# Kernel tuning notes

Hardware: AMD Instinct MI355X
Metric: run time of the kernel (lower is better)

## Reference

```python
import jax, jax.numpy as jnp
import numpy as np

B, N, D = 8, 2048, 256
K = 16384  # codebook_size


def setup_inputs() -> dict:
    key = jax.random.key(0)
    k1, k2, k3, k4 = jax.random.split(key, 4)
    z = jax.random.normal(k1, (B, N, D), dtype=jnp.float32)
    emb_weight = jax.random.normal(k2, (K, D), dtype=jnp.float32) * 0.02
    proj_w = jax.random.normal(k3, (D, D), dtype=jnp.float32) * (1.0 / np.sqrt(D))
    proj_b = jax.random.normal(k4, (D,), dtype=jnp.float32) * 0.01
    return {"z": z, "emb_weight": emb_weight, "proj_w": proj_w, "proj_b": proj_b}


def reference(z, emb_weight, proj_w, proj_b):
    # emb = embedding_proj(embedding.weight)  (torch Linear: x @ W^T + b)
    emb = emb_weight @ proj_w.T + proj_b  # (K, D)
    b, n, d = z.shape
    zf = z.reshape(b * n, d)  # (BN, D)
    # squared euclidean distances: ||z||^2 + ||e||^2 - 2 z e^T
    dist = (
        jnp.sum(zf * zf, axis=1, keepdims=True)
        + jnp.sum(emb * emb, axis=1)
        - 2.0 * jnp.einsum("bd,kd->bk", zf, emb)
    )  # (BN, K)
    q_indices = jnp.argmin(dist, axis=1)  # (BN,) int
    quantized = emb[q_indices].reshape(z.shape)  # (B, N, D)
    # straight-through estimator
    quantized = z + jax.lax.stop_gradient(quantized - z)
    q_indices = q_indices.reshape(b, n)
    # (unregularized_z, emb, regularized_z, bottleneck_rep)
    return z, emb, quantized, q_indices
```

## Files before the change

kernel.cpp:

```cpp
#include <hip/hip_runtime.h>
#include <hip/hip_bf16.h>

#define D      256
#define KCB    16384
#define BNROWS 16384
#define NT     4
#define MARGIN 0.15f
#define BIAS   8.0f
#define ZMAX   5.0f
#define EMAX   0.2f

typedef __attribute__((ext_vector_type(4))) int   int4v;
typedef __attribute__((ext_vector_type(4))) float f32x4;
typedef unsigned long long u64;

__device__ __forceinline__ void gload_lds16(const void* g, void* l) {
    __builtin_amdgcn_global_load_lds(
        (const __attribute__((address_space(1))) void*)g,
        (__attribute__((address_space(3))) void*)l, 16, 0, 0);
}

__device__ __forceinline__ unsigned fmap(float f) {
    unsigned u = __float_as_uint(f);
    return (u & 0x80000000u) ? ~u : (u | 0x80000000u);
}

__device__ __forceinline__ signed char q8(float x, float s) {
    return (signed char)__float2int_rn(fminf(fmaxf(x * s, -127.f), 127.f));
}

__global__ __launch_bounds__(256) void zquant_kernel(
    const float* __restrict__ z, signed char* __restrict__ z8)
{
    const int i = blockIdx.x * 256 + threadIdx.x;
    float4 v = ((const float4*)z)[i];
    const float s = 127.0f / ZMAX;
    char4 c;
    c.x = q8(v.x, s); c.y = q8(v.y, s); c.z = q8(v.z, s); c.w = q8(v.w, s);
    ((char4*)z8)[i] = c;
}

__global__ __launch_bounds__(256) void proj_kernel(
    const float* __restrict__ ew, const float* __restrict__ pw,
    const float* __restrict__ pb, float* __restrict__ emb)
{
    __shared__ float Et[64][65];
    __shared__ float Pt[64][65];
    const int tid = threadIdx.x;
    const int tc  = tid & 15, tr = tid >> 4;
    const int k0  = (blockIdx.x >> 2) * 64;
    const int d0  = (blockIdx.x & 3) * 64;

    float acc[4][4];
#pragma unroll
    for (int a = 0; a < 4; ++a)
#pragma unroll
        for (int b = 0; b < 4; ++b) acc[a][b] = 0.f;

    for (int j0 = 0; j0 < 256; j0 += 64) {
        __syncthreads();
#pragma unroll
        for (int i = 0; i < 4; ++i) {
            const int c = i * 256 + tid;
            const int r = c >> 4, c4 = (c & 15) * 4;
            float4 v = *(const float4*)(ew + (size_t)(k0 + r) * 256 + j0 + c4);
            Et[r][c4 + 0] = v.x; Et[r][c4 + 1] = v.y;
            Et[r][c4 + 2] = v.z; Et[r][c4 + 3] = v.w;
            float4 w = *(const float4*)(pw + (size_t)(d0 + r) * 256 + j0 + c4);
            Pt[r][c4 + 0] = w.x; Pt[r][c4 + 1] = w.y;
            Pt[r][c4 + 2] = w.z; Pt[r][c4 + 3] = w.w;
        }
        __syncthreads();
        for (int j = 0; j < 64; ++j) {
            float ev[4], pv[4];
#pragma unroll
            for (int a = 0; a < 4; ++a) ev[a] = Et[tr * 4 + a][j];
#pragma unroll
            for (int b = 0; b < 4; ++b) pv[b] = Pt[tc * 4 + b][j];
#pragma unroll
            for (int a = 0; a < 4; ++a)
#pragma unroll
                for (int b = 0; b < 4; ++b)
                    acc[a][b] = fmaf(ev[a], pv[b], acc[a][b]);
        }
    }

    const float4 bias = *(const float4*)(pb + d0 + tc * 4);
#pragma unroll
    for (int a = 0; a < 4; ++a) {
        float4 o;
        o.x = acc[a][0] + bias.x; o.y = acc[a][1] + bias.y;
        o.z = acc[a][2] + bias.z; o.w = acc[a][3] + bias.w;
        *(float4*)(emb + (size_t)(k0 + tr * 4 + a) * 256 + d0 + tc * 4) = o;
    }
}

__global__ __launch_bounds__(256) void snorm_equant_kernel(
    const float* __restrict__ emb, float* __restrict__ s,
    signed char* __restrict__ e8)
{
    const int tid = threadIdx.x;
    const int row = blockIdx.x * 64 + (tid >> 2);
    const int qd  = tid & 3;
    const size_t base = (size_t)row * 256;
    const float se = 127.0f / EMAX;
    float sq = 0.f;
#pragma unroll
    for (int j = 0; j < 16; ++j) {
        const int off = qd * 4 + j * 16;
        float4 v = *(const float4*)(emb + base + off);
        char4 c;
        c.x = q8(v.x, se); c.y = q8(v.y, se);
        c.z = q8(v.z, se); c.w = q8(v.w, se);
        *(char4*)(e8 + base + off) = c;
        sq = fmaf(v.x, v.x, fmaf(v.y, v.y, fmaf(v.z, v.z, fmaf(v.w, v.w, sq))));
    }
    sq += __shfl_xor(sq, 1);
    sq += __shfl_xor(sq, 2);
    if (qd == 0) s[row] = sq;
}

__global__ __launch_bounds__(512, 4) void argmin_hi_kernel(
    const signed char* __restrict__ z8, const signed char* __restrict__ e8,
    const float* __restrict__ s,
    unsigned* __restrict__ partial1, unsigned* __restrict__ partial2)
{
    __shared__ alignas(16) short A_lds[3 * 4096];
    __shared__ alignas(16) short B_lds[3 * 8192];

    const int tid  = threadIdx.x;
    const int lane = tid & 63;
    const int wid  = tid >> 6;
    const int wz   = wid >> 2;
    const int wc   = wid & 3;
    const int lcol = lane & 15;
    const int rhi  = lane >> 4;

    const int bm = blockIdx.x >> 6;
    const int bn = blockIdx.x & 63;
    const size_t r0 = (size_t)bm * 128;
    const size_t n0 = (size_t)bn * 256;

    const int slot  = (((lcol & 1) * 4 + rhi) ^ ((lcol >> 1) & 7)) << 3;
    const int aoff0 = wz * 2048 + (lcol >> 1) * 64 + slot;
    const int boff0 = wc * 2048 + (lcol >> 1) * 64 + slot;

    auto goff = [](int c) {
        const int l = c >> 3, u = (c & 7) ^ (l & 7);
        return (size_t)(2 * l + (u >> 2)) * 256 + (size_t)(u & 3) * 16;
    };
    const size_t gA  = goff(tid);
    const int    cB0 = wid * 128 + lane;
    const int    cB1 = cB0 + 64;
    const size_t gB0 = goff(cB0);
    const size_t gB1 = goff(cB1);

    short* const aDst  = A_lds + tid * 8;
    short* const bDst0 = B_lds + cB0 * 8;
    short* const bDst1 = B_lds + cB1 * 8;

    const char* const z8B = (const char*)z8 + r0 * 256;
    const char* const e8B = (const char*)e8 + n0 * 256;

    gload_lds16(z8B + gA, aDst);
    gload_lds16(e8B + gB0, bDst0);
    gload_lds16(e8B + gB1, bDst1);
    gload_lds16(z8B + 64 + gA, aDst + 4096);
    gload_lds16(e8B + 64 + gB0, bDst0 + 8192);
    gload_lds16(e8B + 64 + gB1, bDst1 + 8192);
    asm volatile("s_waitcnt vmcnt(3)" ::: "memory");
    __builtin_amdgcn_s_barrier();

    int4v acc[4][4];
    const int4v izero = {0, 0, 0, 0};
#pragma unroll
    for (int m = 0; m < 4; ++m)
#pragma unroll
        for (int n = 0; n < 4; ++n) acc[m][n] = izero;

#define TILE_BODY(JL)                                                         \
    {                                                                         \
        const int t  = i3 + (JL);                                             \
        const int tp = t + 2;                                                 \
        int4v bq[4];                                                          \
        _Pragma("unroll")                                                     \
        for (int n = 0; n < 4; ++n)            \
            bq[n] = *(const int4v*)(A_lds + (JL) * 4096 + aoff0 + n * 512);   \
        if (tp < NT) {                                                        \
            const char* Ab = z8B + ((size_t)tp << 6);                         \
            const char* Bb = e8B + ((size_t)tp << 6);                         \
            gload_lds16(Ab + gA, aDst + (((JL) + 2) % 3) * 4096);             \
            gload_lds16(Bb + gB0, bDst0 + (((JL) + 2) % 3) * 8192);           \
            gload_lds16(Bb + gB1, bDst1 + (((JL) + 2) % 3) * 8192);           \
        }                                                                     \
        __builtin_amdgcn_s_setprio(1);                                        \
        _Pragma("unroll")                                                     \
        for (int m = 0; m < 4; ++m) {       \
            const int4v am = *(const int4v*)(B_lds + (JL) * 8192 + boff0 + m * 512); \
            _Pragma("unroll")                                                 \
            for (int n = 0; n < 4; ++n)                                       \
                acc[m][n] = __builtin_amdgcn_mfma_i32_16x16x64_i8(            \
                    am, bq[n], acc[m][n], 0, 0, 0);                           \
        }                                                                     \
        __builtin_amdgcn_s_setprio(0);                                        \
        if (tp < NT)                                                          \
            asm volatile("s_waitcnt vmcnt(3)" ::: "memory");                  \
        else if (t + 1 < NT)                                                  \
            asm volatile("s_waitcnt vmcnt(0)" ::: "memory");                  \
        __builtin_amdgcn_s_barrier();                                         \
    }

    {
        const int i3 = 0;
        TILE_BODY(0)
        TILE_BODY(1)
        TILE_BODY(2)
    }
    {
        const int i3 = 3;
        TILE_BODY(0)
    }
#undef TILE_BODY

    const float FS2 = -2.0f * (ZMAX / 127.0f) * (EMAX / 127.0f);
    float4 s8[4];
#pragma unroll
    for (int mc = 0; mc < 4; ++mc) {
        float4 t = *(const float4*)(s + n0 + wc * 64 + mc * 16 + rhi * 4);
        t.x += BIAS; t.y += BIAS; t.z += BIAS; t.w += BIAS;
        s8[mc] = t;
    }

    u64* cand = (u64*)A_lds;
#pragma unroll
    for (int nz = 0; nz < 4; ++nz) {
        unsigned v[16];
#pragma unroll
        for (int mc = 0; mc < 4; ++mc) {
            const unsigned cb = (unsigned)(wc * 64 + mc * 16 + rhi * 4);
            v[mc * 4 + 0] = (__float_as_uint(fmaf(FS2, (float)acc[mc][nz][0], s8[mc].x)) & 0xFFFFFF00u) | (cb + 0);
            v[mc * 4 + 1] = (__float_as_uint(fmaf(FS2, (float)acc[mc][nz][1], s8[mc].y)) & 0xFFFFFF00u) | (cb + 1);
            v[mc * 4 + 2] = (__float_as_uint(fmaf(FS2, (float)acc[mc][nz][2], s8[mc].z)) & 0xFFFFFF00u) | (cb + 2);
            v[mc * 4 + 3] = (__float_as_uint(fmaf(FS2, (float)acc[mc][nz][3], s8[mc].w)) & 0xFFFFFF00u) | (cb + 3);
        }
        unsigned p1 = min(v[0], v[1]), p2 = max(v[0], v[1]);
#pragma unroll
        for (int i = 1; i < 8; ++i) {
            const unsigned l = min(v[2 * i], v[2 * i + 1]);
            const unsigned h = max(v[2 * i], v[2 * i + 1]);
            const unsigned t = max(p1, l);
            p1 = min(p1, l);
            p2 = min(t, min(p2, h));
        }
#pragma unroll
        for (int mask = 16; mask <= 32; mask <<= 1) {
            const unsigned q1 = __shfl_xor(p1, mask);
            const unsigned q2 = __shfl_xor(p2, mask);
            const unsigned t  = max(p1, q1);
            p1 = min(p1, q1);
            p2 = min(t, min(p2, q2));
        }
        if (rhi == 0) {
            const int row = wz * 64 + nz * 16 + lcol;
            cand[row * 4 + wc] = (u64)p1 | ((u64)p2 << 32);
        }
    }
    __syncthreads();
    if (tid < 128) {
        const u64* c4 = cand + (size_t)tid * 4;
        u64 a = c4[0];
        unsigned p1 = (unsigned)a, p2 = (unsigned)(a >> 32);
#pragma unroll
        for (int w = 1; w < 4; ++w) {
            a = c4[w];
            const unsigned q1 = (unsigned)a, q2 = (unsigned)(a >> 32);
            const unsigned t  = max(p1, q1);
            p1 = min(p1, q1);
            p2 = min(t, min(p2, q2));
        }
        partial1[(size_t)bn * BNROWS + r0 + tid] = p1;
        partial2[(size_t)bn * BNROWS + r0 + tid] = p2;
    }
}

__global__ __launch_bounds__(256) void collect_rescore_kernel(
    const unsigned* __restrict__ partial1, const unsigned* __restrict__ partial2,
    const float* __restrict__ z, const float* __restrict__ emb,
    const float* __restrict__ s, int* __restrict__ qidx)
{
    __shared__ float    wsum[4];
    __shared__ unsigned gsb;
    __shared__ int      nsel;
    __shared__ int      selk[128];

    const int tid = threadIdx.x;
    const int row = blockIdx.x;

    unsigned v = 0xFFFFFFFFu;
    int vbn = 0;
    if (tid < 64)       { v = partial1[(size_t)tid * BNROWS + row];        vbn = tid; }
    else if (tid < 128) { v = partial2[(size_t)(tid - 64) * BNROWS + row]; vbn = tid - 64; }

    if (tid < 64) {
        unsigned g = v;
#pragma unroll
        for (int mm = 1; mm < 64; mm <<= 1) g = min(g, (unsigned)__shfl_xor(g, mm));
        if (tid == 0) { gsb = g; nsel = 0; }
    }
    __syncthreads();

    const float    gf  = __uint_as_float(gsb & 0xFFFFFF00u);
    const unsigned thr = __float_as_uint(gf + MARGIN) | 0xFFu;
    if (tid < 128 && v <= thr) {
        const int i = atomicAdd(&nsel, 1);
        selk[i] = vbn * 256 + (int)(v & 0xFFu);
    }
    __syncthreads();

    const float zd = z[(size_t)row * 256 + tid];
    const int   ns = nsel;
    u64 best = ~0ull;
    for (int i = 0; i < ns; ++i) {
        const int k = selk[i];
        float p = zd * emb[(size_t)k * 256 + tid];
#pragma unroll
        for (int mm = 1; mm < 64; mm <<= 1) p += __shfl_xor(p, mm);
        if ((tid & 63) == 0) wsum[tid >> 6] = p;
        __syncthreads();
        if (tid == 0) {
            const float dot = (wsum[0] + wsum[1]) + (wsum[2] + wsum[3]);
            const float sc  = fmaf(-2.f, dot, s[k]);
            const u64 pk = ((u64)fmap(sc) << 32) | (unsigned)k;
            if (pk < best) best = pk;
        }
        __syncthreads();
    }
    if (tid == 0) qidx[row] = (int)(best & 0xffffffffu);
}

__global__ __launch_bounds__(256) void finalize_kernel(
    const float* __restrict__ z, const float* __restrict__ emb,
    const int* __restrict__ qidx,
    float* __restrict__ outz, float* __restrict__ outq,
    float* __restrict__ outidx)
{
    const int row = blockIdx.x;
    const int d   = threadIdx.x;
    const int k   = qidx[row];
    outz[(size_t)row * D + d] = z[(size_t)row * D + d];
    outq[(size_t)row * D + d] = emb[(size_t)k * D + d];
    if (d == 0) outidx[row] = (float)k;
}

extern "C" void kernel_launch(void* const* d_in, const int* in_sizes, int n_in,
                              void* d_out, int out_size, void* d_ws, size_t ws_size,
                              hipStream_t stream)
{
    const float* z  = (const float*)d_in[0];
    const float* ew = (const float*)d_in[1];
    const float* pw = (const float*)d_in[2];
    const float* pb = (const float*)d_in[3];

    float* out     = (float*)d_out;
    float* out_z   = out;
    float* out_emb = out + (size_t)BNROWS * D;
    float* out_q   = out + 2 * (size_t)BNROWS * D;
    float* out_idx = out + 3 * (size_t)BNROWS * D;

    float*       sbuf = (float*)d_ws;
    int*         qidx = (int*)((char*)d_ws + 65536);
    signed char* z8   = (signed char*)((char*)d_ws + 131072);
    signed char* e8   = (signed char*)out_q;
    unsigned* partial1 = (unsigned*)out_z;
    unsigned* partial2 = (unsigned*)out_z + (size_t)BNROWS * 64;

    zquant_kernel<<<(BNROWS * D) / (256 * 4), 256, 0, stream>>>(z, z8);
    proj_kernel<<<(KCB / 64) * 4, 256, 0, stream>>>(ew, pw, pb, out_emb);
    snorm_equant_kernel<<<KCB / 64, 256, 0, stream>>>(out_emb, sbuf, e8);
    argmin_hi_kernel<<<(BNROWS / 128) * (KCB / 256), 512, 0, stream>>>(
        z8, e8, sbuf, partial1, partial2);
    collect_rescore_kernel<<<BNROWS, 256, 0, stream>>>(
        partial1, partial2, z, out_emb, sbuf, qidx);
    finalize_kernel<<<BNROWS, 256, 0, stream>>>(
        z, out_emb, qidx, out_z, out_q, out_idx);
}
```

Before: 203.8 us.

## Fuse finalize into rescore, parallelize candidate rescoring across waves

Merges the finalize kernel into the collect/rescore kernel so the chosen index is consumed in place and the outputs are written without an extra launch or a qidx round trip. Rescoring now runs one candidate per wavefront with float4 loads and shuffle reductions, instead of a block-wide loop with two barriers per candidate. The biased norms are precomputed once in snorm_equant. The partial buffers move from the output region into workspace, which needs more workspace memory and can no longer overlap with outputs that the fused kernel writes.

Result: faster. 180.5 us (-11.4%).

```diff
diff --git a/kernel.cpp b/kernel.cpp
--- a/kernel.cpp
+++ b/kernel.cpp
@@ -97,7 +97,7 @@
 
 __global__ __launch_bounds__(256) void snorm_equant_kernel(
     const float* __restrict__ emb, float* __restrict__ s,
-    signed char* __restrict__ e8)
+    float* __restrict__ s8b, signed char* __restrict__ e8)
 {
     const int tid = threadIdx.x;
     const int row = blockIdx.x * 64 + (tid >> 2);
@@ -117,12 +117,15 @@
     }
     sq += __shfl_xor(sq, 1);
     sq += __shfl_xor(sq, 2);
-    if (qd == 0) s[row] = sq;
+    if (qd == 0) {
+        s[row]   = sq;
+        s8b[row] = sq + BIAS;
+    }
 }
 
 __global__ __launch_bounds__(512, 4) void argmin_hi_kernel(
     const signed char* __restrict__ z8, const signed char* __restrict__ e8,
-    const float* __restrict__ s,
+    const float* __restrict__ s8b,
     unsigned* __restrict__ partial1, unsigned* __restrict__ partial2)
 {
     __shared__ alignas(16) short A_lds[3 * 4096];
@@ -225,11 +228,8 @@
     const float FS2 = -2.0f * (ZMAX / 127.0f) * (EMAX / 127.0f);
     float4 s8[4];
 #pragma unroll
-    for (int mc = 0; mc < 4; ++mc) {
-        float4 t = *(const float4*)(s + n0 + wc * 64 + mc * 16 + rhi * 4);
-        t.x += BIAS; t.y += BIAS; t.z += BIAS; t.w += BIAS;
-        s8[mc] = t;
-    }
+    for (int mc = 0; mc < 4; ++mc)
+        s8[mc] = *(const float4*)(s8b + n0 + wc * 64 + mc * 16 + rhi * 4);
 
     u64* cand = (u64*)A_lds;
 #pragma unroll
@@ -286,15 +286,20 @@
 __global__ __launch_bounds__(256) void collect_rescore_kernel(
     const unsigned* __restrict__ partial1, const unsigned* __restrict__ partial2,
     const float* __restrict__ z, const float* __restrict__ emb,
-    const float* __restrict__ s, int* __restrict__ qidx)
-{
-    __shared__ float    wsum[4];
+    const float* __restrict__ s,
+    float* __restrict__ outz, float* __restrict__ outq,
+    float* __restrict__ outidx)
+{
     __shared__ unsigned gsb;
     __shared__ int      nsel;
     __shared__ int      selk[128];
-
-    const int tid = threadIdx.x;
-    const int row = blockIdx.x;
+    __shared__ u64      wbest[4];
+    __shared__ int      kfin;
+
+    const int tid  = threadIdx.x;
+    const int row  = blockIdx.x;
+    const int lane = tid & 63;
+    const int wid  = tid >> 6;
 
     unsigned v = 0xFFFFFFFFu;
     int vbn = 0;
@@ -317,39 +322,37 @@
     }
     __syncthreads();
 
-    const float zd = z[(size_t)row * 256 + tid];
-    const int   ns = nsel;
+    const float4 zv = *(const float4*)(z + (size_t)row * 256 + lane * 4);
+    const int ns = nsel;
     u64 best = ~0ull;
-    for (int i = 0; i < ns; ++i) {
+    for (int i = wid; i < ns; i += 4) {
         const int k = selk[i];
-        float p = zd * emb[(size_t)k * 256 + tid];
+        const float4 ev = *(const float4*)(emb + (size_t)k * 256 + lane * 4);
+        float p = zv.x * ev.x;
+        p = fmaf(zv.y, ev.y, p);
+        p = fmaf(zv.z, ev.z, p);
+        p = fmaf(zv.w, ev.w, p);
 #pragma unroll
         for (int mm = 1; mm < 64; mm <<= 1) p += __shfl_xor(p, mm);
-        if ((tid & 63) == 0) wsum[tid >> 6] = p;
-        __syncthreads();
-        if (tid == 0) {
-            const float dot = (wsum[0] + wsum[1]) + (wsum[2] + wsum[3]);
-            const float sc  = fmaf(-2.f, dot, s[k]);
-            const u64 pk = ((u64)fmap(sc) << 32) | (unsigned)k;
-            if (pk < best) best = pk;
-        }
-        __syncthreads();
-    }
-    if (tid == 0) qidx[row] = (int)(best & 0xffffffffu);
-}
-
-__global__ __launch_bounds__(256) void finalize_kernel(
-    const float* __restrict__ z, const float* __restrict__ emb,
-    const int* __restrict__ qidx,
-    float* __restrict__ outz, float* __restrict__ outq,
-    float* __restrict__ outidx)
-{
-    const int row = blockIdx.x;
-    const int d   = threadIdx.x;
-    const int k   = qidx[row];
-    outz[(size_t)row * D + d] = z[(size_t)row * D + d];
-    outq[(size_t)row * D + d] = emb[(size_t)k * D + d];
-    if (d == 0) outidx[row] = (float)k;
+        const float sc = fmaf(-2.f, p, s[k]);
+        const u64 pk = ((u64)fmap(sc) << 32) | (unsigned)k;
+        best = (pk < best) ? pk : best;
+    }
+    if (lane == 0) wbest[wid] = best;
+    __syncthreads();
+    if (tid == 0) {
+        u64 b = wbest[0];
+        if (wbest[1] < b) b = wbest[1];
+        if (wbest[2] < b) b = wbest[2];
+        if (wbest[3] < b) b = wbest[3];
+        kfin = (int)(b & 0xffffffffu);
+        outidx[row] = (float)kfin;
+    }
+    __syncthreads();
+
+    const int k = kfin;
+    outz[(size_t)row * 256 + tid] = z[(size_t)row * 256 + tid];
+    outq[(size_t)row * 256 + tid] = emb[(size_t)k * 256 + tid];
 }
 
 extern "C" void kernel_launch(void* const* d_in, const int* in_sizes, int n_in,
@@ -367,20 +370,18 @@
     float* out_q   = out + 2 * (size_t)BNROWS * D;
     float* out_idx = out + 3 * (size_t)BNROWS * D;
 
-    float*       sbuf = (float*)d_ws;
-    int*         qidx = (int*)((char*)d_ws + 65536);
-    signed char* z8   = (signed char*)((char*)d_ws + 131072);
-    signed char* e8   = (signed char*)out_q;
-    unsigned* partial1 = (unsigned*)out_z;
-    unsigned* partial2 = (unsigned*)out_z + (size_t)BNROWS * 64;
+    float*       sbuf  = (float*)d_ws;
+    float*       s8b   = (float*)((char*)d_ws + 65536);
+    signed char* z8    = (signed char*)((char*)d_ws + 131072);
+    unsigned*    part1 = (unsigned*)((char*)d_ws + 131072 + 4194304);
+    unsigned*    part2 = (unsigned*)((char*)d_ws + 131072 + 2 * 4194304);
+    signed char* e8    = (signed char*)out_q;
 
     zquant_kernel<<<(BNROWS * D) / (256 * 4), 256, 0, stream>>>(z, z8);
     proj_kernel<<<(KCB / 64) * 4, 256, 0, stream>>>(ew, pw, pb, out_emb);
-    snorm_equant_kernel<<<KCB / 64, 256, 0, stream>>>(out_emb, sbuf, e8);
+    snorm_equant_kernel<<<KCB / 64, 256, 0, stream>>>(out_emb, sbuf, s8b, e8);
     argmin_hi_kernel<<<(BNROWS / 128) * (KCB / 256), 512, 0, stream>>>(
-        z8, e8, sbuf, partial1, partial2);
+        z8, e8, s8b, part1, part2);
     collect_rescore_kernel<<<BNROWS, 256, 0, stream>>>(
-        partial1, partial2, z, out_emb, sbuf, qidx);
-    finalize_kernel<<<BNROWS, 256, 0, stream>>>(
-        z, out_emb, qidx, out_z, out_q, out_idx);
-}
+        part1, part2, z, out_emb, sbuf, out_z, out_q, out_idx);
+}
```
